# Performance work log

Measured on AMD Instinct MI355X. Metric: run time of the kernel, lower is better.

## Reference

```python
import jax, jax.numpy as jnp
import numpy as np

N = 100000
E = 3200000
IN_C, NHID, OUT_C, K = 256, 128, 40, 2


def gcn_norm(src, dst, ew, n):
    # add self loops with weight 1.0 (PyG gcn_norm default, add_self_loops=True)
    loop = jnp.arange(n, dtype=src.dtype)
    src = jnp.concatenate([src, loop])
    dst = jnp.concatenate([dst, loop])
    ew = jnp.concatenate([ew, jnp.ones((n,), dtype=ew.dtype)])
    deg = jax.ops.segment_sum(ew, dst, num_segments=n)
    dinv = jnp.where(deg > 0, jax.lax.rsqrt(deg), 0.0)
    norm = dinv[src] * ew * dinv[dst]
    return src, dst, norm


def sgconv(x, src, dst, norm, W, b, k, n):
    # x' = (D^-1/2 (A+I) D^-1/2)^k x, then linear
    for _ in range(k):
        x = jax.ops.segment_sum(x[src] * norm[:, None], dst, num_segments=n)
    return x @ W + b


def setup_inputs() -> dict:
    key = jax.random.key(0)
    ks = jax.random.split(key, 8)
    x = jax.random.normal(ks[0], (N, IN_C), dtype=jnp.float32)
    edge_index = jax.random.randint(ks[1], (2, E), 0, N, dtype=jnp.int64)
    edge_weight = jax.random.uniform(ks[2], (E,), dtype=jnp.float32)
    s1 = 1.0 / np.sqrt(IN_C)
    s2 = 1.0 / np.sqrt(NHID)
    W1 = jax.random.uniform(ks[3], (IN_C, NHID), minval=-s1, maxval=s1, dtype=jnp.float32)
    b1 = jax.random.uniform(ks[4], (NHID,), minval=-s1, maxval=s1, dtype=jnp.float32)
    W2 = jax.random.uniform(ks[5], (NHID, OUT_C), minval=-s2, maxval=s2, dtype=jnp.float32)
    b2 = jax.random.uniform(ks[6], (OUT_C,), minval=-s2, maxval=s2, dtype=jnp.float32)
    return {"x": x, "edge_index": edge_index, "edge_weight": edge_weight,
            "W1": W1, "b1": b1, "W2": W2, "b2": b2}


def reference(x, edge_index, edge_weight, W1, b1, W2, b2):
    n = x.shape[0]
    src, dst, norm = gcn_norm(edge_index[0], edge_index[1], edge_weight, n)
    h = jax.nn.relu(sgconv(x, src, dst, norm, W1, b1, K, n))
    # dropout is identity in eval mode (training=False)
    out = sgconv(h, src, dst, norm, W2, b2, K, n)
    return jax.nn.log_softmax(out, axis=1)
```

## Files before the change

### kernel.cpp

```cpp
#include <hip/hip_runtime.h>
#include <math.h>


constexpr int IN_C = 256, NHID = 128, OUT_C = 40;
constexpr int BSHIFT = 7;
constexpr int BCAP = 8064;
constexpr int MAXB = 800;
typedef unsigned int u32;
typedef unsigned short u16;
typedef __attribute__((ext_vector_type(8))) short bf16x8;
typedef __attribute__((ext_vector_type(4))) float f32x4;

__device__ inline u16 f2bf(float f) {
    u32 u = __float_as_uint(f);
    return (u16)((u + 0x7FFF + ((u >> 16) & 1)) >> 16);
}
__device__ inline float sx8(u32 v) { return (float)(int)(signed char)(v & 0xFF); }

__global__ __launch_bounds__(256) void k_bucketize(const int* __restrict__ src,
                                                   const int* __restrict__ dst,
                                                   const float* __restrict__ ew,
                                                   int* __restrict__ bcur,
                                                   int2* __restrict__ bbuf,
                                                   int E, int nbins) {
    __shared__ int hist[MAXB];
    __shared__ int base[MAXB];
    int tid = threadIdx.x;
    int chunk = (E + gridDim.x - 1) / gridDim.x;
    int e0 = blockIdx.x * chunk;
    int e1 = min(E, e0 + chunk);
    for (int i = tid; i < nbins; i += 256) hist[i] = 0;
    __syncthreads();
    for (int e = e0 + tid; e < e1; e += 256)
        atomicAdd(&hist[dst[e] >> BSHIFT], 1);
    __syncthreads();
    for (int i = tid; i < nbins; i += 256) {
        int c = hist[i];
        base[i] = c ? atomicAdd(&bcur[i], c) : 0;
        hist[i] = 0;
    }
    __syncthreads();
    for (int e = e0 + tid; e < e1; e += 256) {
        int d = dst[e];
        int b = d >> BSHIFT;
        int r = atomicAdd(&hist[b], 1);
        int pos = base[b] + r;
        if (pos < BCAP) {
            int meta = src[e] | ((d & 127) << 17);
            bbuf[(size_t)b * BCAP + pos] = make_int2(meta, __float_as_int(ew[e]));
        }
    }
}

__global__ __launch_bounds__(256) void k_bcnt_deg(const int2* __restrict__ bbuf,
                                                  const int* __restrict__ bcur,
                                                  int* __restrict__ cnt,
                                                  float* __restrict__ dinv,
                                                  float* __restrict__ selfnorm, int N) {
    __shared__ int hist[128];
    __shared__ float dsum[128];
    int b = blockIdx.x;
    int tid = threadIdx.x;
    if (tid < 128) { hist[tid] = 0; dsum[tid] = 0.f; }
    __syncthreads();
    int c = min(bcur[b], BCAP);
    const int2* p = bbuf + (size_t)b * BCAP;
    for (int e = tid; e < c; e += 256) {
        int2 rec = p[e];
        int dl = rec.x >> 17;
        atomicAdd(&hist[dl], 1);
        atomicAdd(&dsum[dl], __int_as_float(rec.y));
    }
    __syncthreads();
    int node = b * 128 + tid;
    if (tid < 128 && node < N) {
        cnt[node] = hist[tid];
        float d = dsum[tid] + 1.0f;
        dinv[node] = rsqrtf(d);
        selfnorm[node] = 1.0f / d;
    }
}

__global__ __launch_bounds__(256) void k_scan_part(const int* __restrict__ cnt,
                                                   int* __restrict__ partial, int N) {
    __shared__ int sh[256];
    int i = blockIdx.x * 256 + threadIdx.x;
    sh[threadIdx.x] = (i < N) ? cnt[i] : 0;
    __syncthreads();
    for (int off = 128; off > 0; off >>= 1) {
        if (threadIdx.x < off) sh[threadIdx.x] += sh[threadIdx.x + off];
        __syncthreads();
    }
    if (threadIdx.x == 0) partial[blockIdx.x] = sh[0];
}

__global__ __launch_bounds__(512) void k_scan_top(int* __restrict__ partial, int nb) {
    __shared__ int sh[512];
    int t = threadIdx.x;
    int v = (t < nb) ? partial[t] : 0;
    sh[t] = v;
    __syncthreads();
    for (int off = 1; off < 512; off <<= 1) {
        int add = (t >= off) ? sh[t - off] : 0;
        __syncthreads();
        sh[t] += add;
        __syncthreads();
    }
    if (t < nb) partial[t] = sh[t] - v;
}

__global__ __launch_bounds__(256) void k_scan_apply(const int* __restrict__ cnt,
                                                    const int* __restrict__ partial,
                                                    int* __restrict__ row_start, int N) {
    __shared__ int sh[256];
    int i = blockIdx.x * 256 + threadIdx.x;
    int v = (i < N) ? cnt[i] : 0;
    sh[threadIdx.x] = v;
    __syncthreads();
    for (int off = 1; off < 256; off <<= 1) {
        int add = (threadIdx.x >= off) ? sh[threadIdx.x - off] : 0;
        __syncthreads();
        sh[threadIdx.x] += add;
        __syncthreads();
    }
    if (i < N) row_start[i] = sh[threadIdx.x] - v + partial[blockIdx.x];
}

__global__ __launch_bounds__(256) void k_place(const int2* __restrict__ bbuf,
                                               const int* __restrict__ bcur,
                                               const int* __restrict__ row_start,
                                               const float* __restrict__ dinv,
                                               int2* __restrict__ csr, int N) {
    __shared__ int rs[128];
    __shared__ int cur[128];
    __shared__ float dv[128];
    int b = blockIdx.x;
    int tid = threadIdx.x;
    int node = b * 128 + tid;
    if (tid < 128) {
        rs[tid] = (node < N) ? row_start[node] : 0;
        dv[tid] = (node < N) ? dinv[node] : 0.f;
        cur[tid] = 0;
    }
    __syncthreads();
    int c = min(bcur[b], BCAP);
    const int2* p = bbuf + (size_t)b * BCAP;
    for (int e = tid; e < c; e += 256) {
        int2 rec = p[e];
        int dl = rec.x >> 17;
        int s = rec.x & 0x1FFFF;
        float w = dinv[s] * __int_as_float(rec.y) * dv[dl];
        int r = atomicAdd(&cur[dl], 1);
        csr[rs[dl] + r] = make_int2(s, __float_as_int(w));
    }
}

__global__ __launch_bounds__(256) void k_wconv(const float* __restrict__ W,
                                               u16* __restrict__ Wc) {
    int o = blockIdx.x * 256 + threadIdx.x;
    if (o < IN_C * NHID) {
        int j = o & 7, col = (o >> 3) & 127, c = o >> 10;
        Wc[o] = f2bf(W[(size_t)(c * 8 + j) * NHID + col]);
    }
}

__global__ __launch_bounds__(256) void k_gemm1(const float* __restrict__ X,
                                               const u16* __restrict__ Wc,
                                               u32* __restrict__ Yq,
                                               float* __restrict__ Ys, int N) {
    int tid = threadIdx.x;
    int wv = tid >> 6, lane = tid & 63;
    int q = lane >> 4, r16 = lane & 15;
    int row = blockIdx.x * 64 + wv * 16 + r16;
    int rowc = min(row, N - 1);
    const float* xp = X + (size_t)rowc * IN_C + q * 8;
    f32x4 acc[8];
#pragma unroll
    for (int i = 0; i < 8; ++i) acc[i] = (f32x4){0.f, 0.f, 0.f, 0.f};
#pragma unroll
    for (int ks = 0; ks < 8; ++ks) {
        float4 a0 = *(const float4*)(xp + ks * 32);
        float4 a1 = *(const float4*)(xp + ks * 32 + 4);
        bf16x8 xf;
        xf[0] = (short)f2bf(a0.x); xf[1] = (short)f2bf(a0.y);
        xf[2] = (short)f2bf(a0.z); xf[3] = (short)f2bf(a0.w);
        xf[4] = (short)f2bf(a1.x); xf[5] = (short)f2bf(a1.y);
        xf[6] = (short)f2bf(a1.z); xf[7] = (short)f2bf(a1.w);
        int c = ks * 4 + q;
#pragma unroll
        for (int ct = 0; ct < 8; ++ct) {
            bf16x8 wf = *(const bf16x8*)&Wc[(size_t)((c << 7) + ct * 16 + r16) << 3];
            acc[ct] = __builtin_amdgcn_mfma_f32_16x16x32_bf16(wf, xf, acc[ct], 0, 0, 0);
        }
    }
    float m = 0.f;
#pragma unroll
    for (int ct = 0; ct < 8; ++ct) {
        m = fmaxf(m, fmaxf(fmaxf(fabsf(acc[ct].x), fabsf(acc[ct].y)),
                           fmaxf(fabsf(acc[ct].z), fabsf(acc[ct].w))));
    }
    m = fmaxf(m, __shfl_xor(m, 16, 64));
    m = fmaxf(m, __shfl_xor(m, 32, 64));
    float qs = m > 0.f ? 127.0f / m : 0.f;
    if (row < N) {
        u32* yp = Yq + (size_t)row * 32;
#pragma unroll
        for (int ct = 0; ct < 8; ++ct) {
            int q0 = (int)rintf(acc[ct].x * qs);
            int q1 = (int)rintf(acc[ct].y * qs);
            int q2 = (int)rintf(acc[ct].z * qs);
            int q3 = (int)rintf(acc[ct].w * qs);
            yp[ct * 4 + q] = (q0 & 0xFF) | ((q1 & 0xFF) << 8) | ((q2 & 0xFF) << 16) | ((q3 & 0xFF) << 24);
        }
        if (lane < 16) Ys[row] = m * (1.0f / 127.0f);
    }
}

__global__ __launch_bounds__(256) void k_gemm2(const u32* __restrict__ Hq,
                                               const float* __restrict__ Hs,
                                               const float* __restrict__ W2,
                                               const float* __restrict__ b1,
                                               u16* __restrict__ Tq,
                                               float* __restrict__ Ts, int N) {
    __shared__ float Ws[NHID * OUT_C];
    __shared__ float As[64][132];
    int tid = threadIdx.x;
    for (int idx = tid; idx < NHID * OUT_C; idx += 256) Ws[idx] = W2[idx];
    int bm = blockIdx.x * 64;
#pragma unroll
    for (int j = 0; j < 8; ++j) {
        int idx = tid + j * 256;
        int r = idx >> 5, c = (idx & 31) * 4;
        int grow = bm + r;
        float4 v = make_float4(0.f, 0.f, 0.f, 0.f);
        if (grow < N) {
            u32 w = Hq[(size_t)grow * 32 + (idx & 31)];
            float s = Hs[grow];
            v = make_float4(s * sx8(w), s * sx8(w >> 8), s * sx8(w >> 16), s * sx8(w >> 24));
        }
        v.x = fmaxf(v.x + b1[c + 0], 0.f);
        v.y = fmaxf(v.y + b1[c + 1], 0.f);
        v.z = fmaxf(v.z + b1[c + 2], 0.f);
        v.w = fmaxf(v.w + b1[c + 3], 0.f);
        *(float4*)&As[r][c] = v;
    }
    __syncthreads();
    int r = tid >> 2;
    int c0 = (tid & 3) * 10;
    float acc[10] = {};
#pragma unroll 4
    for (int k = 0; k < NHID; ++k) {
        float a = As[r][k];
#pragma unroll
        for (int j = 0; j < 10; ++j) acc[j] += a * Ws[k * OUT_C + c0 + j];
    }
    float m = 0.f;
#pragma unroll
    for (int j = 0; j < 10; ++j) m = fmaxf(m, fabsf(acc[j]));
    m = fmaxf(m, __shfl_xor(m, 1, 64));
    m = fmaxf(m, __shfl_xor(m, 2, 64));
    float qs = m > 0.f ? 127.0f / m : 0.f;
    int grow = bm + r;
    if (grow < N) {
        u16* tp = Tq + (size_t)grow * 20 + (tid & 3) * 5;
#pragma unroll
        for (int j = 0; j < 5; ++j) {
            int q0 = (int)rintf(acc[2 * j] * qs);
            int q1 = (int)rintf(acc[2 * j + 1] * qs);
            tp[j] = (u16)((q0 & 0xFF) | ((q1 & 0xFF) << 8));
        }
        if ((tid & 3) == 0) Ts[grow] = m * (1.0f / 127.0f);
    }
}

__global__ __launch_bounds__(256) void k_prop128(const u16* __restrict__ in,
                                                 const float* __restrict__ ins,
                                                 u16* __restrict__ outq,
                                                 float* __restrict__ outs,
                                                 const int2* __restrict__ csr,
                                                 const int* __restrict__ row_start,
                                                 const int* __restrict__ cnt,
                                                 const float* __restrict__ selfnorm, int N) {
    int wid = (blockIdx.x * 256 + threadIdx.x) >> 6;
    int lane = threadIdx.x & 63;
    if (wid >= N) return;
    int beg = row_start[wid], num = cnt[wid];
    float ssc = selfnorm[wid] * ins[0 + wid < N ? wid : 0];
    ssc = selfnorm[wid] * ins[wid];
    u32 xv = in[(size_t)wid * 64 + lane];
    float ax = ssc * sx8(xv), ay = ssc * sx8(xv >> 8);
    float bx = 0.f, by = 0.f;
    int e = beg, end = beg + num;
    while (e < end) {
        int m = min(64, end - e);
        int2 rec = csr[e + min(lane, m - 1)];
        int j = 0;
        for (; j + 4 <= m; j += 4) {
            int s0 = __shfl(rec.x, j, 64);     float w0 = __int_as_float(__shfl(rec.y, j, 64)) * ins[s0];
            int s1 = __shfl(rec.x, j + 1, 64); float w1 = __int_as_float(__shfl(rec.y, j + 1, 64)) * ins[s1];
            int s2 = __shfl(rec.x, j + 2, 64); float w2 = __int_as_float(__shfl(rec.y, j + 2, 64)) * ins[s2];
            int s3 = __shfl(rec.x, j + 3, 64); float w3 = __int_as_float(__shfl(rec.y, j + 3, 64)) * ins[s3];
            u32 x0 = in[(size_t)s0 * 64 + lane];
            u32 x1 = in[(size_t)s1 * 64 + lane];
            u32 x2 = in[(size_t)s2 * 64 + lane];
            u32 x3 = in[(size_t)s3 * 64 + lane];
            ax += w0 * sx8(x0); ay += w0 * sx8(x0 >> 8);
            bx += w1 * sx8(x1); by += w1 * sx8(x1 >> 8);
            ax += w2 * sx8(x2); ay += w2 * sx8(x2 >> 8);
            bx += w3 * sx8(x3); by += w3 * sx8(x3 >> 8);
        }
        for (; j < m; ++j) {
            int s0 = __shfl(rec.x, j, 64);
            float w0 = __int_as_float(__shfl(rec.y, j, 64)) * ins[s0];
            u32 x0 = in[(size_t)s0 * 64 + lane];
            ax += w0 * sx8(x0); ay += w0 * sx8(x0 >> 8);
        }
        e += m;
    }
    ax += bx; ay += by;
    float m2 = fmaxf(fabsf(ax), fabsf(ay));
#pragma unroll
    for (int o = 32; o > 0; o >>= 1) m2 = fmaxf(m2, __shfl_xor(m2, o, 64));
    float qs = m2 > 0.f ? 127.0f / m2 : 0.f;
    int qx = (int)rintf(ax * qs), qy = (int)rintf(ay * qs);
    outq[(size_t)wid * 64 + lane] = (u16)((qx & 0xFF) | ((qy & 0xFF) << 8));
    if (lane == 0) outs[wid] = m2 * (1.0f / 127.0f);
}

__global__ __launch_bounds__(256) void k_prop40(const u16* __restrict__ in,
                                                const float* __restrict__ ins,
                                                u16* __restrict__ outq,
                                                float* __restrict__ outs,
                                                const int2* __restrict__ csr,
                                                const int* __restrict__ row_start,
                                                const int* __restrict__ cnt,
                                                const float* __restrict__ selfnorm, int N) {
    int wid = (blockIdx.x * 256 + threadIdx.x) >> 6;
    int lane = threadIdx.x & 63;
    if (wid >= N) return;
    int half = lane >> 5, fl = lane & 31;
    bool act = fl < 20;
    int beg = row_start[wid], end = beg + cnt[wid];
    float ax = 0.f, ay = 0.f, bx = 0.f, by = 0.f;
    if (act && half == 0) {
        u32 u = in[(size_t)wid * 20 + fl];
        float ssc = selfnorm[wid] * ins[wid];
        ax = ssc * sx8(u); ay = ssc * sx8(u >> 8);
    }
    int e = beg;
    while (e < end) {
        int m = min(64, end - e);
        int2 rec = csr[e + min(lane, m - 1)];
        int j = half;
        for (; j + 2 < m; j += 4) {
            int s0 = __shfl(rec.x, j, 64);     float w0 = __int_as_float(__shfl(rec.y, j, 64)) * ins[s0];
            int s1 = __shfl(rec.x, j + 2, 64); float w1 = __int_as_float(__shfl(rec.y, j + 2, 64)) * ins[s1];
            if (act) {
                u32 u0 = in[(size_t)s0 * 20 + fl];
                u32 u1 = in[(size_t)s1 * 20 + fl];
                ax += w0 * sx8(u0); ay += w0 * sx8(u0 >> 8);
                bx += w1 * sx8(u1); by += w1 * sx8(u1 >> 8);
            }
        }
        for (; j < m; j += 2) {
            int s0 = __shfl(rec.x, j, 64);
            float w0 = __int_as_float(__shfl(rec.y, j, 64)) * ins[s0];
            if (act) {
                u32 u0 = in[(size_t)s0 * 20 + fl];
                ax += w0 * sx8(u0); ay += w0 * sx8(u0 >> 8);
            }
        }
        e += m;
    }
    ax += bx; ay += by;
    ax += __shfl_xor(ax, 32, 64);
    ay += __shfl_xor(ay, 32, 64);
    float m2 = fmaxf(fabsf(ax), fabsf(ay));
#pragma unroll
    for (int o = 16; o > 0; o >>= 1) m2 = fmaxf(m2, __shfl_xor(m2, o, 64));
    float qs = m2 > 0.f ? 127.0f / m2 : 0.f;
    if (half == 0 && act) {
        int qx = (int)rintf(ax * qs), qy = (int)rintf(ay * qs);
        outq[(size_t)wid * 20 + fl] = (u16)((qx & 0xFF) | ((qy & 0xFF) << 8));
        if (fl == 0) outs[wid] = m2 * (1.0f / 127.0f);
    }
}

__global__ __launch_bounds__(256) void k_prop40_lsm(const u16* __restrict__ in,
                                                    const float* __restrict__ ins,
                                                    float* __restrict__ out,
                                                    const int2* __restrict__ csr,
                                                    const int* __restrict__ row_start,
                                                    const int* __restrict__ cnt,
                                                    const float* __restrict__ selfnorm,
                                                    const float* __restrict__ b2, int N) {
    int wid = (blockIdx.x * 256 + threadIdx.x) >> 6;
    int lane = threadIdx.x & 63;
    if (wid >= N) return;
    int half = lane >> 5, fl = lane & 31;
    bool act = fl < 20;
    int beg = row_start[wid], end = beg + cnt[wid];
    float ax = 0.f, ay = 0.f, bx = 0.f, by = 0.f;
    if (act && half == 0) {
        u32 u = in[(size_t)wid * 20 + fl];
        float ssc = selfnorm[wid] * ins[wid];
        ax = ssc * sx8(u); ay = ssc * sx8(u >> 8);
    }
    int e = beg;
    while (e < end) {
        int m = min(64, end - e);
        int2 rec = csr[e + min(lane, m - 1)];
        int j = half;
        for (; j + 2 < m; j += 4) {
            int s0 = __shfl(rec.x, j, 64);     float w0 = __int_as_float(__shfl(rec.y, j, 64)) * ins[s0];
            int s1 = __shfl(rec.x, j + 2, 64); float w1 = __int_as_float(__shfl(rec.y, j + 2, 64)) * ins[s1];
            if (act) {
                u32 u0 = in[(size_t)s0 * 20 + fl];
                u32 u1 = in[(size_t)s1 * 20 + fl];
                ax += w0 * sx8(u0); ay += w0 * sx8(u0 >> 8);
                bx += w1 * sx8(u1); by += w1 * sx8(u1 >> 8);
            }
        }
        for (; j < m; j += 2) {
            int s0 = __shfl(rec.x, j, 64);
            float w0 = __int_as_float(__shfl(rec.y, j, 64)) * ins[s0];
            if (act) {
                u32 u0 = in[(size_t)s0 * 20 + fl];
                ax += w0 * sx8(u0); ay += w0 * sx8(u0 >> 8);
            }
        }
        e += m;
    }
    ax += bx; ay += by;
    ax += __shfl_xor(ax, 32, 64);
    ay += __shfl_xor(ay, 32, 64);
    float vx = -INFINITY, vy = -INFINITY;
    if (half == 0 && act) {
        vx = ax + b2[2 * fl];
        vy = ay + b2[2 * fl + 1];
    }
    float m2 = fmaxf(vx, vy);
#pragma unroll
    for (int o = 32; o > 0; o >>= 1) m2 = fmaxf(m2, __shfl_xor(m2, o, 64));
    float ex = (half == 0 && act) ? (__expf(vx - m2) + __expf(vy - m2)) : 0.f;
    float s = ex;
#pragma unroll
    for (int o = 32; o > 0; o >>= 1) s += __shfl_xor(s, o, 64);
    if (half == 0 && act) {
        float ls = logf(s);
        float2 o2 = make_float2(vx - m2 - ls, vy - m2 - ls);
        *(float2*)&out[(size_t)wid * 40 + 2 * fl] = o2;
    }
}

extern "C" void kernel_launch(void* const* d_in, const int* in_sizes, int n_in,
                              void* d_out, int out_size, void* d_ws, size_t ws_size,
                              hipStream_t stream) {
    const int N = in_sizes[0] / IN_C;
    const int E = in_sizes[2];
    const float* x  = (const float*)d_in[0];
    const int*   src = (const int*)d_in[1];
    const int*   dst = src + E;
    const float* ew = (const float*)d_in[2];
    const float* W1 = (const float*)d_in[3];
    const float* b1 = (const float*)d_in[4];
    const float* W2 = (const float*)d_in[5];
    const float* b2 = (const float*)d_in[6];
    float* out = (float*)d_out;

    char* p = (char*)d_ws;
    auto alloc = [&](size_t bytes) -> char* {
        char* r = p;
        p += (bytes + 255) & ~(size_t)255;
        return r;
    };
    float* dinv     = (float*)alloc((size_t)N * 4);
    float* selfnorm = (float*)alloc((size_t)N * 4);
    int*   cnt      = (int*)alloc((size_t)N * 4);
    int*   row_start= (int*)alloc((size_t)N * 4);
    int*   partial  = (int*)alloc(((N + 255) / 256) * 4);
    int*   bcur     = (int*)alloc(MAXB * 4);
    u16*   Wc       = (u16*)alloc((size_t)IN_C * NHID * 2);
    int2*  csr      = (int2*)alloc((size_t)E * 8);
    const int nbins = (N + 127) >> BSHIFT;
    char*  region   = alloc((size_t)nbins * BCAP * 8);
    int2*  bbuf = (int2*)region;
    u16*   h8A  = (u16*)(region);
    u16*   h8B  = (u16*)(region + 13000000);
    u16*   t8A  = (u16*)(region + 26000000);
    u16*   t8B  = (u16*)(region + 30200000);
    float* sA   = (float*)(region + 34400000);
    float* sB   = (float*)(region + 34900000);
    float* tsA  = (float*)(region + 35400000);
    float* tsB  = (float*)(region + 35900000);

    hipMemsetAsync(bcur, 0, nbins * 4, stream);

    int gn = (N + 255) / 256;
    int nb = gn;
    int gp = (N + 3) / 4;

    k_bucketize<<<256, 256, 0, stream>>>(src, dst, ew, bcur, bbuf, E, nbins);
    k_bcnt_deg<<<nbins, 256, 0, stream>>>(bbuf, bcur, cnt, dinv, selfnorm, N);
    k_scan_part<<<nb, 256, 0, stream>>>(cnt, partial, N);
    k_scan_top<<<1, 512, 0, stream>>>(partial, nb);
    k_scan_apply<<<nb, 256, 0, stream>>>(cnt, partial, row_start, N);
    k_place<<<nbins, 256, 0, stream>>>(bbuf, bcur, row_start, dinv, csr, N);
    k_wconv<<<(IN_C * NHID + 255) / 256, 256, 0, stream>>>(W1, Wc);

    k_gemm1<<<(N + 63) / 64, 256, 0, stream>>>(x, Wc, (u32*)h8A, sA, N);

    k_prop128<<<gp, 256, 0, stream>>>(h8A, sA, h8B, sB, csr, row_start, cnt, selfnorm, N);
    k_prop128<<<gp, 256, 0, stream>>>(h8B, sB, h8A, sA, csr, row_start, cnt, selfnorm, N);

    k_gemm2<<<(N + 63) / 64, 256, 0, stream>>>((const u32*)h8A, sA, W2, b1, t8A, tsA, N);

    k_prop40<<<gp, 256, 0, stream>>>(t8A, tsA, t8B, tsB, csr, row_start, cnt, selfnorm, N);
    k_prop40_lsm<<<gp, 256, 0, stream>>>(t8B, tsB, out, csr, row_start, cnt, selfnorm, b2, N);
}
```

Measured before the change: 544.7 us.

## Stage CSR records in LDS, pad 40-ch rows to 64B, unroll gathers by 8

Edge records for each 64-edge chunk are staged in shared memory instead of being broadcast with per-edge shuffles, and the 128-channel gather loop is unrolled to 8 outstanding loads. The int8 40-channel intermediate rows are padded from 40 to 64 bytes so each gathered row is aligned. The two 40-channel propagation kernels now share a common body. These changes aim to cut shuffle overhead and raise memory-level parallelism, at the cost of more register pressure and a larger intermediate buffer (region offsets are moved to fit it).

```diff
diff --git a/kernel.cpp b/kernel.cpp
--- a/kernel.cpp
+++ b/kernel.cpp
@@ -262,7 +262,7 @@
     float qs = m > 0.f ? 127.0f / m : 0.f;
     int grow = bm + r;
     if (grow < N) {
-        u16* tp = Tq + (size_t)grow * 20 + (tid & 3) * 5;
+        u16* tp = Tq + (size_t)grow * 32 + (tid & 3) * 5;
 #pragma unroll
         for (int j = 0; j < 5; ++j) {
             int q0 = (int)rintf(acc[2 * j] * qs);
@@ -281,39 +281,61 @@
                                                  const int* __restrict__ row_start,
                                                  const int* __restrict__ cnt,
                                                  const float* __restrict__ selfnorm, int N) {
-    int wid = (blockIdx.x * 256 + threadIdx.x) >> 6;
-    int lane = threadIdx.x & 63;
+    __shared__ int2 stage[256];
+    int tid = threadIdx.x;
+    int wid = (blockIdx.x * 256 + tid) >> 6;
+    int lane = tid & 63;
+    int wb = tid & ~63;
     if (wid >= N) return;
     int beg = row_start[wid], num = cnt[wid];
-    float ssc = selfnorm[wid] * ins[0 + wid < N ? wid : 0];
-    ssc = selfnorm[wid] * ins[wid];
+    float ssc = selfnorm[wid] * ins[wid];
     u32 xv = in[(size_t)wid * 64 + lane];
     float ax = ssc * sx8(xv), ay = ssc * sx8(xv >> 8);
     float bx = 0.f, by = 0.f;
     int e = beg, end = beg + num;
     while (e < end) {
         int m = min(64, end - e);
-        int2 rec = csr[e + min(lane, m - 1)];
+        stage[wb + lane] = csr[e + min(lane, m - 1)];
         int j = 0;
-        for (; j + 4 <= m; j += 4) {
-            int s0 = __shfl(rec.x, j, 64);     float w0 = __int_as_float(__shfl(rec.y, j, 64)) * ins[s0];
-            int s1 = __shfl(rec.x, j + 1, 64); float w1 = __int_as_float(__shfl(rec.y, j + 1, 64)) * ins[s1];
-            int s2 = __shfl(rec.x, j + 2, 64); float w2 = __int_as_float(__shfl(rec.y, j + 2, 64)) * ins[s2];
-            int s3 = __shfl(rec.x, j + 3, 64); float w3 = __int_as_float(__shfl(rec.y, j + 3, 64)) * ins[s3];
-            u32 x0 = in[(size_t)s0 * 64 + lane];
-            u32 x1 = in[(size_t)s1 * 64 + lane];
-            u32 x2 = in[(size_t)s2 * 64 + lane];
-            u32 x3 = in[(size_t)s3 * 64 + lane];
+        for (; j + 8 <= m; j += 8) {
+            int2 r0 = stage[wb + j + 0];
+            int2 r1 = stage[wb + j + 1];
+            int2 r2 = stage[wb + j + 2];
+            int2 r3 = stage[wb + j + 3];
+            int2 r4 = stage[wb + j + 4];
+            int2 r5 = stage[wb + j + 5];
+            int2 r6 = stage[wb + j + 6];
+            int2 r7 = stage[wb + j + 7];
+            float w0 = __int_as_float(r0.y) * ins[r0.x];
+            float w1 = __int_as_float(r1.y) * ins[r1.x];
+            float w2 = __int_as_float(r2.y) * ins[r2.x];
+            float w3 = __int_as_float(r3.y) * ins[r3.x];
+            float w4 = __int_as_float(r4.y) * ins[r4.x];
+            float w5 = __int_as_float(r5.y) * ins[r5.x];
+            float w6 = __int_as_float(r6.y) * ins[r6.x];
+            float w7 = __int_as_float(r7.y) * ins[r7.x];
+            u32 x0 = in[(size_t)r0.x * 64 + lane];
+            u32 x1 = in[(size_t)r1.x * 64 + lane];
+            u32 x2 = in[(size_t)r2.x * 64 + lane];
+            u32 x3 = in[(size_t)r3.x * 64 + lane];
+            u32 x4 = in[(size_t)r4.x * 64 + lane];
+            u32 x5 = in[(size_t)r5.x * 64 + lane];
+            u32 x6 = in[(size_t)r6.x * 64 + lane];
+            u32 x7 = in[(size_t)r7.x * 64 + lane];
             ax += w0 * sx8(x0); ay += w0 * sx8(x0 >> 8);
             bx += w1 * sx8(x1); by += w1 * sx8(x1 >> 8);
             ax += w2 * sx8(x2); ay += w2 * sx8(x2 >> 8);
             bx += w3 * sx8(x3); by += w3 * sx8(x3 >> 8);
+            ax += w4 * sx8(x4); ay += w4 * sx8(x4 >> 8);
+            bx += w5 * sx8(x5); by += w5 * sx8(x5 >> 8);
+            ax += w6 * sx8(x6); ay += w6 * sx8(x6 >> 8);
+            bx += w7 * sx8(x7); by += w7 * sx8(x7 >> 8);
         }
         for (; j < m; ++j) {
-            int s0 = __shfl(rec.x, j, 64);
-            float w0 = __int_as_float(__shfl(rec.y, j, 64)) * ins[s0];
-            u32 x0 = in[(size_t)s0 * 64 + lane];
-            ax += w0 * sx8(x0); ay += w0 * sx8(x0 >> 8);
+            int2 r = stage[wb + j];
+            float w = __int_as_float(r.y) * ins[r.x];
+            u32 x = in[(size_t)r.x * 64 + lane];
+            ax += w * sx8(x); ay += w * sx8(x >> 8);
         }
         e += m;
     }
@@ -325,6 +347,65 @@
     int qx = (int)rintf(ax * qs), qy = (int)rintf(ay * qs);
     outq[(size_t)wid * 64 + lane] = (u16)((qx & 0xFF) | ((qy & 0xFF) << 8));
     if (lane == 0) outs[wid] = m2 * (1.0f / 127.0f);
+}
+
+__device__ inline void prop40_body(const u16* __restrict__ in,
+                                   const float* __restrict__ ins,
+                                   const int2* __restrict__ csr,
+                                   const int* __restrict__ row_start,
+                                   const int* __restrict__ cnt,
+                                   const float* __restrict__ selfnorm,
+                                   int2* stage, int wb,
+                                   int wid, int lane, int N,
+                                   float& axo, float& ayo) {
+    int half = lane >> 5, fl = lane & 31;
+    bool act = fl < 20;
+    int beg = row_start[wid], end = beg + cnt[wid];
+    float ax = 0.f, ay = 0.f, bx = 0.f, by = 0.f;
+    if (act && half == 0) {
+        u32 u = in[(size_t)wid * 32 + fl];
+        float ssc = selfnorm[wid] * ins[wid];
+        ax = ssc * sx8(u); ay = ssc * sx8(u >> 8);
+    }
+    int e = beg;
+    while (e < end) {
+        int m = min(64, end - e);
+        stage[wb + lane] = csr[e + min(lane, m - 1)];
+        int j = 0;
+        for (; j + 8 <= m; j += 8) {
+            int2 r0 = stage[wb + j + half];
+            int2 r1 = stage[wb + j + 2 + half];
+            int2 r2 = stage[wb + j + 4 + half];
+            int2 r3 = stage[wb + j + 6 + half];
+            float w0 = __int_as_float(r0.y) * ins[r0.x];
+            float w1 = __int_as_float(r1.y) * ins[r1.x];
+            float w2 = __int_as_float(r2.y) * ins[r2.x];
+            float w3 = __int_as_float(r3.y) * ins[r3.x];
+            if (act) {
+                u32 u0 = in[(size_t)r0.x * 32 + fl];
+                u32 u1 = in[(size_t)r1.x * 32 + fl];
+                u32 u2 = in[(size_t)r2.x * 32 + fl];
+                u32 u3 = in[(size_t)r3.x * 32 + fl];
+                ax += w0 * sx8(u0); ay += w0 * sx8(u0 >> 8);
+                bx += w1 * sx8(u1); by += w1 * sx8(u1 >> 8);
+                ax += w2 * sx8(u2); ay += w2 * sx8(u2 >> 8);
+                bx += w3 * sx8(u3); by += w3 * sx8(u3 >> 8);
+            }
+        }
+        for (; j + half < m; j += 2) {
+            int2 r = stage[wb + j + half];
+            float w = __int_as_float(r.y) * ins[r.x];
+            if (act) {
+                u32 u = in[(size_t)r.x * 32 + fl];
+                ax += w * sx8(u); ay += w * sx8(u >> 8);
+            }
+        }
+        e += m;
+    }
+    ax += bx; ay += by;
+    ax += __shfl_xor(ax, 32, 64);
+    ay += __shfl_xor(ay, 32, 64);
+    axo = ax; ayo = ay;
 }
 
 __global__ __launch_bounds__(256) void k_prop40(const u16* __restrict__ in,
@@ -335,53 +416,22 @@
                                                 const int* __restrict__ row_start,
                                                 const int* __restrict__ cnt,
                                                 const float* __restrict__ selfnorm, int N) {
-    int wid = (blockIdx.x * 256 + threadIdx.x) >> 6;
-    int lane = threadIdx.x & 63;
+    __shared__ int2 stage[256];
+    int tid = threadIdx.x;
+    int wid = (blockIdx.x * 256 + tid) >> 6;
+    int lane = tid & 63;
     if (wid >= N) return;
+    float ax, ay;
+    prop40_body(in, ins, csr, row_start, cnt, selfnorm, stage, tid & ~63, wid, lane, N, ax, ay);
     int half = lane >> 5, fl = lane & 31;
-    bool act = fl < 20;
-    int beg = row_start[wid], end = beg + cnt[wid];
-    float ax = 0.f, ay = 0.f, bx = 0.f, by = 0.f;
-    if (act && half == 0) {
-        u32 u = in[(size_t)wid * 20 + fl];
-        float ssc = selfnorm[wid] * ins[wid];
-        ax = ssc * sx8(u); ay = ssc * sx8(u >> 8);
-    }
-    int e = beg;
-    while (e < end) {
-        int m = min(64, end - e);
-        int2 rec = csr[e + min(lane, m - 1)];
-        int j = half;
-        for (; j + 2 < m; j += 4) {
-            int s0 = __shfl(rec.x, j, 64);     float w0 = __int_as_float(__shfl(rec.y, j, 64)) * ins[s0];
-            int s1 = __shfl(rec.x, j + 2, 64); float w1 = __int_as_float(__shfl(rec.y, j + 2, 64)) * ins[s1];
-            if (act) {
-                u32 u0 = in[(size_t)s0 * 20 + fl];
-                u32 u1 = in[(size_t)s1 * 20 + fl];
-                ax += w0 * sx8(u0); ay += w0 * sx8(u0 >> 8);
-                bx += w1 * sx8(u1); by += w1 * sx8(u1 >> 8);
-            }
-        }
-        for (; j < m; j += 2) {
-            int s0 = __shfl(rec.x, j, 64);
-            float w0 = __int_as_float(__shfl(rec.y, j, 64)) * ins[s0];
-            if (act) {
-                u32 u0 = in[(size_t)s0 * 20 + fl];
-                ax += w0 * sx8(u0); ay += w0 * sx8(u0 >> 8);
-            }
-        }
-        e += m;
-    }
-    ax += bx; ay += by;
-    ax += __shfl_xor(ax, 32, 64);
-    ay += __shfl_xor(ay, 32, 64);
     float m2 = fmaxf(fabsf(ax), fabsf(ay));
+    if (fl >= 20) m2 = 0.f;
 #pragma unroll
     for (int o = 16; o > 0; o >>= 1) m2 = fmaxf(m2, __shfl_xor(m2, o, 64));
     float qs = m2 > 0.f ? 127.0f / m2 : 0.f;
-    if (half == 0 && act) {
+    if (half == 0 && fl < 20) {
         int qx = (int)rintf(ax * qs), qy = (int)rintf(ay * qs);
-        outq[(size_t)wid * 20 + fl] = (u16)((qx & 0xFF) | ((qy & 0xFF) << 8));
+        outq[(size_t)wid * 32 + fl] = (u16)((qx & 0xFF) | ((qy & 0xFF) << 8));
         if (fl == 0) outs[wid] = m2 * (1.0f / 127.0f);
     }
 }
@@ -394,46 +444,15 @@
                                                     const int* __restrict__ cnt,
                                                     const float* __restrict__ selfnorm,
                                                     const float* __restrict__ b2, int N) {
-    int wid = (blockIdx.x * 256 + threadIdx.x) >> 6;
-    int lane = threadIdx.x & 63;
+    __shared__ int2 stage[256];
+    int tid = threadIdx.x;
+    int wid = (blockIdx.x * 256 + tid) >> 6;
+    int lane = tid & 63;
     if (wid >= N) return;
+    float ax, ay;
+    prop40_body(in, ins, csr, row_start, cnt, selfnorm, stage, tid & ~63, wid, lane, N, ax, ay);
     int half = lane >> 5, fl = lane & 31;
     bool act = fl < 20;
-    int beg = row_start[wid], end = beg + cnt[wid];
-    float ax = 0.f, ay = 0.f, bx = 0.f, by = 0.f;
-    if (act && half == 0) {
-        u32 u = in[(size_t)wid * 20 + fl];
-        float ssc = selfnorm[wid] * ins[wid];
-        ax = ssc * sx8(u); ay = ssc * sx8(u >> 8);
-    }
-    int e = beg;
-    while (e < end) {
-        int m = min(64, end - e);
-        int2 rec = csr[e + min(lane, m - 1)];
-        int j = half;
-        for (; j + 2 < m; j += 4) {
-            int s0 = __shfl(rec.x, j, 64);     float w0 = __int_as_float(__shfl(rec.y, j, 64)) * ins[s0];
-            int s1 = __shfl(rec.x, j + 2, 64); float w1 = __int_as_float(__shfl(rec.y, j + 2, 64)) * ins[s1];
-            if (act) {
-                u32 u0 = in[(size_t)s0 * 20 + fl];
-                u32 u1 = in[(size_t)s1 * 20 + fl];
-                ax += w0 * sx8(u0); ay += w0 * sx8(u0 >> 8);
-                bx += w1 * sx8(u1); by += w1 * sx8(u1 >> 8);
-            }
-        }
-        for (; j < m; j += 2) {
-            int s0 = __shfl(rec.x, j, 64);
-            float w0 = __int_as_float(__shfl(rec.y, j, 64)) * ins[s0];
-            if (act) {
-                u32 u0 = in[(size_t)s0 * 20 + fl];
-                ax += w0 * sx8(u0); ay += w0 * sx8(u0 >> 8);
-            }
-        }
-        e += m;
-    }
-    ax += bx; ay += by;
-    ax += __shfl_xor(ax, 32, 64);
-    ay += __shfl_xor(ay, 32, 64);
     float vx = -INFINITY, vy = -INFINITY;
     if (half == 0 && act) {
         vx = ax + b2[2 * fl];
@@ -488,11 +507,11 @@
     u16*   h8A  = (u16*)(region);
     u16*   h8B  = (u16*)(region + 13000000);
     u16*   t8A  = (u16*)(region + 26000000);
-    u16*   t8B  = (u16*)(region + 30200000);
-    float* sA   = (float*)(region + 34400000);
-    float* sB   = (float*)(region + 34900000);
-    float* tsA  = (float*)(region + 35400000);
-    float* tsB  = (float*)(region + 35900000);
+    u16*   t8B  = (u16*)(region + 33000000);
+    float* sA   = (float*)(region + 40000000);
+    float* sB   = (float*)(region + 40500000);
+    float* tsA  = (float*)(region + 41000000);
+    float* tsB  = (float*)(region + 41500000);
 
     hipMemsetAsync(bcur, 0, nbins * 4, stream);
 
```

Result: faster. 529.3 us (-2.8%).
